# Kernel optimization log

Hardware: AMD Instinct MI355X
Metric: run time of the kernel (lower is better)

The kernel has to match this reference:

```python
import jax, jax.numpy as jnp
import numpy as np

B, T, D, H = 64, 512, 128, 512


def setup_inputs() -> dict:
    key = jax.random.key(0)
    ks = jax.random.split(key, 16)
    s_d = 1.0 / np.sqrt(D)
    s_h = 1.0 / np.sqrt(H)
    inp = {"x": jax.random.normal(ks[0], (B, T, D), dtype=jnp.float32)}
    # W* : [H, D] with bias; U* : [H, H] no bias (matches nn.Linear layout)
    inp["Wi_w"] = jax.random.uniform(ks[1], (H, D), minval=-s_d, maxval=s_d)
    inp["Wi_b"] = jax.random.uniform(ks[2], (H,), minval=-s_d, maxval=s_d)
    inp["Ui_w"] = jax.random.uniform(ks[3], (H, H), minval=-s_h, maxval=s_h)
    inp["Wf_w"] = jax.random.uniform(ks[4], (H, D), minval=-s_d, maxval=s_d)
    inp["Wf_b"] = jax.random.uniform(ks[5], (H,), minval=-s_d, maxval=s_d)
    inp["Uf_w"] = jax.random.uniform(ks[6], (H, H), minval=-s_h, maxval=s_h)
    inp["Wo_w"] = jax.random.uniform(ks[7], (H, D), minval=-s_d, maxval=s_d)
    inp["Wo_b"] = jax.random.uniform(ks[8], (H,), minval=-s_d, maxval=s_d)
    inp["Uo_w"] = jax.random.uniform(ks[9], (H, H), minval=-s_h, maxval=s_h)
    inp["Wg_w"] = jax.random.uniform(ks[10], (H, D), minval=-s_d, maxval=s_d)
    inp["Wg_b"] = jax.random.uniform(ks[11], (H,), minval=-s_d, maxval=s_d)
    inp["Ug_w"] = jax.random.uniform(ks[12], (H, H), minval=-s_h, maxval=s_h)
    inp["out_w"] = jax.random.uniform(ks[13], (1, H), minval=-s_h, maxval=s_h)
    inp["out_b"] = jnp.zeros((1,), dtype=jnp.float32)
    return inp


def _lstm_forward(x, Wi_w, Wi_b, Ui_w, Wf_w, Wf_b, Uf_w, Wo_w, Wo_b, Uo_w,
                  Wg_w, Wg_b, Ug_w, out_w, out_b):
    Bb = x.shape[0]
    Hh = Ui_w.shape[0]
    uf_d = jnp.diagonal(Uf_w)
    ui_d = jnp.diagonal(Ui_w)
    ug_d = jnp.diagonal(Ug_w)
    # Precompute input-side projections for all timesteps: [T, B, H]
    xi = (jnp.einsum('btd,hd->bth', x, Wi_w) + Wi_b).transpose(1, 0, 2)
    xf = (jnp.einsum('btd,hd->bth', x, Wf_w) + Wf_b).transpose(1, 0, 2)
    xo = (jnp.einsum('btd,hd->bth', x, Wo_w) + Wo_b).transpose(1, 0, 2)
    xg = (jnp.einsum('btd,hd->bth', x, Wg_w) + Wg_b).transpose(1, 0, 2)

    def step(carry, inp_t):
        h, c_prev = carry
        xi_t, xf_t, xo_t, xg_t = inp_t
        i = jax.nn.sigmoid(xi_t + h @ Ui_w.T)
        f = jax.nn.sigmoid(xf_t + h @ Uf_w.T)
        o = jax.nn.sigmoid(xo_t + h @ Uo_w.T)
        g = jnp.tanh(xg_t + h @ Ug_w.T)  # ln disabled -> identity
        c = f * c_prev + i * g
        tanh_c = jnp.tanh(c)
        h_new = o * tanh_c
        y = h_new @ out_w.T + out_b
        e = o * (1.0 - tanh_c ** 2)
        cdiag = (c_prev * (f * (1.0 - f)) * uf_d
                 + i * (1.0 - g ** 2) * ug_d
                 + g * (i * (1.0 - i)) * ui_d)
        return (h_new, c), (y, h_new, f, e, cdiag)

    h0 = jnp.zeros((Bb, Hh), dtype=x.dtype)
    c0 = jnp.zeros((Bb, Hh), dtype=x.dtype)
    _, (ys, hs, fs, es, cds) = jax.lax.scan(step, (h0, c0), (xi, xf, xo, xg))
    # scan outputs are time-major [T, B, ...] -> [B, T, ...]
    to_bt = lambda a: a.transpose(1, 0, 2)
    return to_bt(ys), to_bt(hs), to_bt(fs), to_bt(es), to_bt(cds)


def reference(x, Wi_w, Wi_b, Ui_w, Wf_w, Wf_b, Uf_w, Wo_w, Wo_b, Uo_w,
              Wg_w, Wg_b, Ug_w, out_w, out_b):
    return _lstm_forward(x, Wi_w, Wi_b, Ui_w, Wf_w, Wf_b, Uf_w, Wo_w, Wo_b,
                         Uo_w, Wg_w, Wg_b, Ug_w, out_w, out_b)
```

## Files before the change

### kernel.cpp

```cpp
#include <hip/hip_runtime.h>
#include <math.h>

#define BB 64
#define TT 512
#define DD 128
#define HH 512
#define NROW 16
#define NCG 16
#define NWG 256
#define TAGM 511u

#define LOADB2(d0,d1, ptr)                                                    \
  asm volatile("global_load_dword %0, %2, off sc0 sc1\n\t"                    \
               "global_load_dword %1, %2, off offset:2048 sc0 sc1"            \
               : "=v"(d0), "=v"(d1) : "v"(ptr) : "memory")

#define BARRIER_LGKM() asm volatile("s_waitcnt lgkmcnt(0)\n\ts_barrier" ::: "memory")

__global__ __launch_bounds__(256) void uT2_kernel(
    const float* __restrict__ Ui_w, const float* __restrict__ Uf_w,
    const float* __restrict__ Uo_w, const float* __restrict__ Ug_w,
    float* __restrict__ utT2)
{
    const int cg = blockIdx.x;
    for (int idx = threadIdx.x; idx < HH * 128; idx += 256) {
        const int k = idx >> 7, ii = idx & 127;
        const int l = ii >> 1, d = ii & 1;
        const int j = cg * 32 + (l & 31);
        const int g = ((l >> 5) << 1) + d;
        const float* U = (g == 0) ? Ui_w : (g == 1) ? Uf_w : (g == 2) ? Uo_w : Ug_w;
        utT2[((size_t)cg * HH + k) * 128 + ii] = U[(size_t)j * HH + k];
    }
}

__global__ __launch_bounds__(512, 2) void lstm_persist(
    const float* __restrict__ utT2,
    const float* __restrict__ Ui_w, const float* __restrict__ Uf_w,
    const float* __restrict__ Ug_w,
    const float* __restrict__ x,
    const float* __restrict__ Wi_w, const float* __restrict__ Wi_b,
    const float* __restrict__ Wf_w, const float* __restrict__ Wf_b,
    const float* __restrict__ Wo_w, const float* __restrict__ Wo_b,
    const float* __restrict__ Wg_w, const float* __restrict__ Wg_b,
    float* __restrict__ b_i, float* __restrict__ b_f,
    float* __restrict__ b_o, float* __restrict__ b_g,
    unsigned* __restrict__ hpub,
    int* __restrict__ flags)
{
    __shared__ float  hlds[8][4][64];
    __shared__ float2 red2[2][8][2][128];
    __shared__ float  xps[2][4][128];
    __shared__ float  shout[2][4][128];
    __shared__ float  xlds[2][4][128];

    const int tid  = threadIdx.x;
    const int w    = tid >> 6;
    const int lane = tid & 63;
    const int wg   = blockIdx.x;
    const int r    = wg & 15;
    const int cg   = wg >> 4;
    const int k0   = w << 6;

    float2 u2[64];
    {
        const float* ub = utT2 + ((size_t)cg * HH + k0) * 128 + 2 * lane;
        #pragma unroll
        for (int k = 0; k < 64; ++k) u2[k] = *(const float2*)(ub + (size_t)k * 128);
    }

    float creg = 0.f, uid = 0.f, ufd = 0.f, ugd = 0.f;
    int jjg = 0, gb = 0;
    if (tid < 128) {
        jjg = cg * 32 + (tid & 31);
        gb  = r * 4 + (tid >> 5);
        uid = Ui_w[(size_t)jjg * HH + jjg];
        ufd = Uf_w[(size_t)jjg * HH + jjg];
        ugd = Ug_w[(size_t)jjg * HH + jjg];
    }

    float4 wreg[16];
    float  wbias = 0.f;
    const int ga = (w >= 4) ? (w - 4) : 0;
    if (w >= 4) {
        const int col = lane & 31, dh = lane >> 5;
        const float* Ws = (ga == 0) ? Wi_w : (ga == 1) ? Wf_w : (ga == 2) ? Wo_w : Wg_w;
        const float* Bs = (ga == 0) ? Wi_b : (ga == 1) ? Wf_b : (ga == 2) ? Wo_b : Wg_b;
        const float* base = Ws + (size_t)(cg * 32 + col) * DD + dh * 64;
        #pragma unroll
        for (int k4 = 0; k4 < 16; ++k4) wreg[k4] = *(const float4*)(base + k4 * 4);
        wbias = Bs[cg * 32 + col];
    }

    if (w == 4) {
        const int bx = lane >> 4, c8 = lane & 15;
        #pragma unroll
        for (int u = 0; u < 2; ++u) {
            const float* xs = x + ((size_t)(r * 4 + bx) * TT + u) * DD + c8 * 8;
            *(float4*)&xlds[u][bx][c8 * 8]     = *(const float4*)(xs);
            *(float4*)&xlds[u][bx][c8 * 8 + 4] = *(const float4*)(xs + 4);
        }
    }
    __syncthreads();
    if (w >= 4) {
        const int col = lane & 31, dh = lane >> 5;
        #pragma unroll
        for (int b = 0; b < 4; ++b) {
            float a = 0.f;
            #pragma unroll
            for (int k4 = 0; k4 < 16; ++k4) {
                const float4 xv = *(const float4*)&xlds[0][b][dh * 64 + k4 * 4];
                const float4 ww = wreg[k4];
                a = fmaf(xv.x, ww.x, a); a = fmaf(xv.y, ww.y, a);
                a = fmaf(xv.z, ww.z, a); a = fmaf(xv.w, ww.w, a);
            }
            const float full = a + __shfl_xor(a, 32);
            if (lane < 32) xps[0][ga][b * 32 + col] = full + wbias;
        }
    }
    __syncthreads();

    for (int t = 0; t < TT; ++t) {
        const int p  = t & 1;
        const int np = p ^ 1;
        const unsigned tg = (unsigned)t & TAGM;

        unsigned hv[4];
        const char* hb = (const char*)hpub
                       + ((size_t)(p * 64 + r * 4) * HH + k0 + lane) * 4;
        for (;;) {
            LOADB2(hv[0], hv[1], hb);
            LOADB2(hv[2], hv[3], hb + 4096);
            asm volatile("s_waitcnt vmcnt(0)" ::: "memory");
            __builtin_amdgcn_sched_barrier(0);
            unsigned bad = 0;
            #pragma unroll
            for (int b = 0; b < 4; ++b) bad |= (hv[b] ^ tg) & TAGM;
            if (__all(bad == 0)) break;
            const int* fb = &flags[p * (NROW * NCG) + r * NCG];
            for (;;) {
                const int fv = __hip_atomic_load(&fb[lane & 15], __ATOMIC_RELAXED,
                                                 __HIP_MEMORY_SCOPE_AGENT);
                if (__all(fv >= t)) break;
                __builtin_amdgcn_s_sleep(2);
            }
        }

        #pragma unroll
        for (int b = 0; b < 4; ++b)
            hlds[w][b][lane] = __uint_as_float(hv[b] & ~TAGM);

        float acc[4][2];
        #pragma unroll
        for (int b = 0; b < 4; ++b) { acc[b][0] = 0.f; acc[b][1] = 0.f; }
        #pragma unroll
        for (int k4 = 0; k4 < 16; ++k4) {
            #pragma unroll
            for (int b = 0; b < 4; ++b) {
                const float4 h4 = *(const float4*)&hlds[w][b][k4 * 4];
                const float2 ua = u2[k4 * 4 + 0];
                const float2 ub = u2[k4 * 4 + 1];
                const float2 uc = u2[k4 * 4 + 2];
                const float2 ud = u2[k4 * 4 + 3];
                acc[b][0] = fmaf(h4.x, ua.x, acc[b][0]);
                acc[b][1] = fmaf(h4.x, ua.y, acc[b][1]);
                acc[b][0] = fmaf(h4.y, ub.x, acc[b][0]);
                acc[b][1] = fmaf(h4.y, ub.y, acc[b][1]);
                acc[b][0] = fmaf(h4.z, uc.x, acc[b][0]);
                acc[b][1] = fmaf(h4.z, uc.y, acc[b][1]);
                acc[b][0] = fmaf(h4.w, ud.x, acc[b][0]);
                acc[b][1] = fmaf(h4.w, ud.y, acc[b][1]);
            }
        }
        {
            const int col = lane & 31, gp = lane >> 5;
            #pragma unroll
            for (int b = 0; b < 4; ++b)
                red2[p][w][gp][b * 32 + col] = make_float2(acc[b][0], acc[b][1]);
        }
        BARRIER_LGKM();

        if (w < 2) {
            float s0 = 0.f, s1 = 0.f, s2 = 0.f, s3 = 0.f;
            #pragma unroll
            for (int ww = 0; ww < 8; ++ww) {
                const float2 a = red2[p][ww][0][tid];
                const float2 b = red2[p][ww][1][tid];
                s0 += a.x; s1 += a.y; s2 += b.x; s3 += b.y;
            }
            const float pi = xps[p][0][tid] + s0;
            const float pf = xps[p][1][tid] + s1;
            const float po = xps[p][2][tid] + s2;
            const float pg = xps[p][3][tid] + s3;

            const float ig = __fdividef(1.f, 1.f + __expf(-pi));
            const float fg = __fdividef(1.f, 1.f + __expf(-pf));
            const float og = __fdividef(1.f, 1.f + __expf(-po));
            const float tgg = __expf(-2.f * fmaxf(pg, -40.f));
            const float gg = __fdividef(1.f - tgg, 1.f + tgg);

            const float cp = creg;
            const float c  = fg * cp + ig * gg;
            creg = c;
            const float tc = __expf(-2.f * fmaxf(c, -40.f));
            const float th = __fdividef(1.f - tc, 1.f + tc);
            const float h  = og * th;
            const float e  = og * (1.f - th * th);
            const float cd = cp * (fg * (1.f - fg)) * ufd
                           + ig * (1.f - gg * gg) * ugd
                           + gg * (ig * (1.f - ig)) * uid;

            const unsigned pk = (__float_as_uint(h) & ~TAGM)
                              | ((unsigned)(t + 1) & TAGM);
            unsigned* dp = hpub + ((size_t)np * 64 + gb) * HH + jjg;
            asm volatile("global_store_dword %0, %1, off sc0 sc1"
                         :: "v"(dp), "v"(pk) : "memory");
            if (tid == 0)
                __hip_atomic_store(&flags[np * (NROW * NCG) + r * NCG + cg], t + 1,
                                   __ATOMIC_RELAXED, __HIP_MEMORY_SCOPE_AGENT);

            shout[p][0][tid] = h;
            shout[p][1][tid] = fg;
            shout[p][2][tid] = e;
            shout[p][3][tid] = cd;
        } else if (w < 4) {
            if (t > 0) {
                const int a2  = ((w - 2) << 1) | (lane >> 5);
                const int i32 = lane & 31;
                float* dstb = (a2 == 0) ? b_i : (a2 == 1) ? b_f
                            : (a2 == 2) ? b_o : b_g;
                const float4 v = *(const float4*)&shout[np][a2][i32 * 4];
                *(float4*)(dstb + ((size_t)(r * 4 + (i32 >> 3)) * TT + (t - 1)) * HH
                           + cg * 32 + (i32 & 7) * 4) = v;
            }
        } else {
            if (t + 1 < TT) {
                const int col = lane & 31, dh = lane >> 5;
                #pragma unroll
                for (int b = 0; b < 4; ++b) {
                    float a = 0.f;
                    #pragma unroll
                    for (int k4 = 0; k4 < 16; ++k4) {
                        const float4 xv = *(const float4*)&xlds[np][b][dh * 64 + k4 * 4];
                        const float4 ww = wreg[k4];
                        a = fmaf(xv.x, ww.x, a); a = fmaf(xv.y, ww.y, a);
                        a = fmaf(xv.z, ww.z, a); a = fmaf(xv.w, ww.w, a);
                    }
                    const float full = a + __shfl_xor(a, 32);
                    if (lane < 32) xps[np][ga][b * 32 + col] = full + wbias;
                }
            }
            if (w == 4 && t + 2 < TT) {
                const int bx = lane >> 4, c8 = lane & 15;
                const float* xs = x + ((size_t)(r * 4 + bx) * TT + (t + 2)) * DD + c8 * 8;
                *(float4*)&xlds[p][bx][c8 * 8]     = *(const float4*)(xs);
                *(float4*)&xlds[p][bx][c8 * 8 + 4] = *(const float4*)(xs + 4);
            }
        }
    }

    __syncthreads();
    if (w == 2 || w == 3) {
        const int a2  = ((w - 2) << 1) | (lane >> 5);
        const int i32 = lane & 31;
        float* dstb = (a2 == 0) ? b_i : (a2 == 1) ? b_f : (a2 == 2) ? b_o : b_g;
        const float4 v = *(const float4*)&shout[1][a2][i32 * 4];
        *(float4*)(dstb + ((size_t)(r * 4 + (i32 >> 3)) * TT + (TT - 1)) * HH
                   + cg * 32 + (i32 & 7) * 4) = v;
    }
}

__global__ __launch_bounds__(256) void lstm_y(
    const float* __restrict__ hs, const float* __restrict__ out_w,
    const float* __restrict__ out_b, float* __restrict__ ys)
{
    const int wave = threadIdx.x >> 6;
    const int lane = threadIdx.x & 63;
    const int rr = blockIdx.x * 4 + wave;

    const float4* hv = (const float4*)(hs + (size_t)rr * HH);
    const float4* wv = (const float4*)out_w;
    float acc = 0.f;
    #pragma unroll
    for (int i = 0; i < 2; ++i) {
        float4 h4 = hv[lane * 2 + i];
        float4 w4 = wv[lane * 2 + i];
        acc += h4.x * w4.x + h4.y * w4.y + h4.z * w4.z + h4.w * w4.w;
    }
    #pragma unroll
    for (int m = 32; m >= 1; m >>= 1) acc += __shfl_xor(acc, m, 64);
    if (lane == 0) ys[rr] = acc + out_b[0];
}

extern "C" void kernel_launch(void* const* d_in, const int* in_sizes, int n_in,
                              void* d_out, int out_size, void* d_ws, size_t ws_size,
                              hipStream_t stream)
{
    const float* x    = (const float*)d_in[0];
    const float* Wi_w = (const float*)d_in[1];
    const float* Wi_b = (const float*)d_in[2];
    const float* Ui_w = (const float*)d_in[3];
    const float* Wf_w = (const float*)d_in[4];
    const float* Wf_b = (const float*)d_in[5];
    const float* Uf_w = (const float*)d_in[6];
    const float* Wo_w = (const float*)d_in[7];
    const float* Wo_b = (const float*)d_in[8];
    const float* Uo_w = (const float*)d_in[9];
    const float* Wg_w = (const float*)d_in[10];
    const float* Wg_b = (const float*)d_in[11];
    const float* Ug_w = (const float*)d_in[12];
    const float* out_w = (const float*)d_in[13];
    const float* out_b = (const float*)d_in[14];

    float* ys  = (float*)d_out;
    float* hs  = ys + (size_t)BB * TT;
    float* fs  = hs + (size_t)BB * TT * HH;
    float* es  = fs + (size_t)BB * TT * HH;
    float* cds = es + (size_t)BB * TT * HH;

    unsigned* hpub  = (unsigned*)d_ws;
    int*      flags = (int*)(hpub + (size_t)2 * BB * HH);
    float*    utT2  = (float*)(flags + 2 * NROW * NCG);

    hipMemsetAsync(d_ws, 0,
                   (size_t)2 * BB * HH * sizeof(unsigned)
                   + (size_t)2 * NROW * NCG * sizeof(int), stream);

    uT2_kernel<<<NCG, 256, 0, stream>>>(Ui_w, Uf_w, Uo_w, Ug_w, utT2);

    lstm_persist<<<NWG, 512, 0, stream>>>(utT2, Ui_w, Uf_w, Ug_w,
                                          x, Wi_w, Wi_b, Wf_w, Wf_b,
                                          Wo_w, Wo_b, Wg_w, Wg_b,
                                          hs, fs, es, cds, hpub, flags);

    lstm_y<<<(BB * TT) / 4, 256, 0, stream>>>(hs, out_w, out_b, ys);
}
```

Before: 3.154 ms.

## Add XCC-local fast path for hidden-state exchange with system-scope fallback

```diff
diff --git a/kernel.cpp b/kernel.cpp
--- a/kernel.cpp
+++ b/kernel.cpp
@@ -9,8 +9,13 @@
 #define NCG 16
 #define NWG 256
 #define TAGM 511u
-
-#define LOADB2(d0,d1, ptr)                                                    \
+#define AG __ATOMIC_RELAXED, __HIP_MEMORY_SCOPE_AGENT
+
+#define LOADF2(d0,d1, ptr)                                                    \
+  asm volatile("global_load_dword %0, %2, off sc0\n\t"                        \
+               "global_load_dword %1, %2, off offset:2048 sc0"                \
+               : "=v"(d0), "=v"(d1) : "v"(ptr) : "memory")
+#define LOADS2(d0,d1, ptr)                                                    \
   asm volatile("global_load_dword %0, %2, off sc0 sc1\n\t"                    \
                "global_load_dword %1, %2, off offset:2048 sc0 sc1"            \
                : "=v"(d0), "=v"(d1) : "v"(ptr) : "memory")
@@ -45,13 +50,15 @@
     float* __restrict__ b_i, float* __restrict__ b_f,
     float* __restrict__ b_o, float* __restrict__ b_g,
     unsigned* __restrict__ hpub,
-    int* __restrict__ flags)
+    unsigned* __restrict__ hpub2,
+    int* __restrict__ hand)
 {
     __shared__ float  hlds[8][4][64];
     __shared__ float2 red2[2][8][2][128];
     __shared__ float  xps[2][4][128];
     __shared__ float  shout[2][4][128];
     __shared__ float  xlds[2][4][128];
+    __shared__ int    fastsh;
 
     const int tid  = threadIdx.x;
     const int w    = tid >> 6;
@@ -66,6 +73,24 @@
         const float* ub = utT2 + ((size_t)cg * HH + k0) * 128 + 2 * lane;
         #pragma unroll
         for (int k = 0; k < 64; ++k) u2[k] = *(const float2*)(ub + (size_t)k * 128);
+    }
+
+    {
+        const int xcc = __builtin_amdgcn_s_getreg(63508) & 0xf;
+        if (tid == 0) {
+            __hip_atomic_store(&hand[2 + wg], 0x100 | xcc, AG);
+            __hip_atomic_fetch_or((unsigned*)&hand[1], 1u << (xcc & 31), AG);
+            __hip_atomic_fetch_add(&hand[0], 1, AG);
+            while (__hip_atomic_load(&hand[0], AG) < NWG)
+                __builtin_amdgcn_s_sleep(8);
+            int ok = (xcc < 8) ? 1 : 0;
+            const int my = 0x100 | xcc;
+            for (int m = 0; m < NCG; ++m)
+                ok &= (__hip_atomic_load(&hand[2 + r + 16 * m], AG) == my) ? 1 : 0;
+            const unsigned msk = (unsigned)__hip_atomic_load(&hand[1], AG);
+            ok &= (__popc(msk) >= 2) ? 1 : 0;
+            fastsh = ok;
+        }
     }
 
     float creg = 0.f, uid = 0.f, ufd = 0.f, ugd = 0.f;
@@ -101,6 +126,8 @@
         }
     }
     __syncthreads();
+    const bool fastp = (fastsh != 0);
+    int mode = fastp ? 0 : 1;
     if (w >= 4) {
         const int col = lane & 31, dh = lane >> 5;
         #pragma unroll
@@ -124,30 +151,46 @@
         const int np = p ^ 1;
         const unsigned tg = (unsigned)t & TAGM;
 
-        unsigned hv[4];
-        const char* hb = (const char*)hpub
-                       + ((size_t)(p * 64 + r * 4) * HH + k0 + lane) * 4;
-        for (;;) {
-            LOADB2(hv[0], hv[1], hb);
-            LOADB2(hv[2], hv[3], hb + 4096);
-            asm volatile("s_waitcnt vmcnt(0)" ::: "memory");
-            __builtin_amdgcn_sched_barrier(0);
-            unsigned bad = 0;
-            #pragma unroll
-            for (int b = 0; b < 4; ++b) bad |= (hv[b] ^ tg) & TAGM;
-            if (__all(bad == 0)) break;
-            const int* fb = &flags[p * (NROW * NCG) + r * NCG];
-            for (;;) {
-                const int fv = __hip_atomic_load(&fb[lane & 15], __ATOMIC_RELAXED,
-                                                 __HIP_MEMORY_SCOPE_AGENT);
-                if (__all(fv >= t)) break;
-                __builtin_amdgcn_s_sleep(2);
-            }
-        }
-
-        #pragma unroll
-        for (int b = 0; b < 4; ++b)
-            hlds[w][b][lane] = __uint_as_float(hv[b] & ~TAGM);
+        if (t == 0) {
+            #pragma unroll
+            for (int b = 0; b < 4; ++b) hlds[w][b][lane] = 0.f;
+        } else {
+            unsigned hv[4];
+            const size_t hoff = ((size_t)(p * 64 + r * 4) * HH + k0 + lane) * 4;
+            bool got = false;
+            if (mode == 0) {
+                const char* hb = (const char*)hpub + hoff;
+                for (int tries = 0; tries < 1024; ++tries) {
+                    LOADF2(hv[0], hv[1], hb);
+                    LOADF2(hv[2], hv[3], hb + 4096);
+                    asm volatile("s_waitcnt vmcnt(0)" ::: "memory");
+                    __builtin_amdgcn_sched_barrier(0);
+                    unsigned bad = 0;
+                    #pragma unroll
+                    for (int b = 0; b < 4; ++b) bad |= (hv[b] ^ tg) & TAGM;
+                    if (__all(bad == 0)) { got = true; break; }
+                    __builtin_amdgcn_s_sleep(1);
+                }
+                if (!got) mode = 1;
+            }
+            if (!got) {
+                const char* hb = (const char*)hpub2 + hoff;
+                for (;;) {
+                    LOADS2(hv[0], hv[1], hb);
+                    LOADS2(hv[2], hv[3], hb + 4096);
+                    asm volatile("s_waitcnt vmcnt(0)" ::: "memory");
+                    __builtin_amdgcn_sched_barrier(0);
+                    unsigned bad = 0;
+                    #pragma unroll
+                    for (int b = 0; b < 4; ++b) bad |= (hv[b] ^ tg) & TAGM;
+                    if (__all(bad == 0)) break;
+                    __builtin_amdgcn_s_sleep(2);
+                }
+            }
+            #pragma unroll
+            for (int b = 0; b < 4; ++b)
+                hlds[w][b][lane] = __uint_as_float(hv[b] & ~TAGM);
+        }
 
         float acc[4][2];
         #pragma unroll
@@ -180,6 +223,7 @@
         BARRIER_LGKM();
 
         if (w < 2) {
+            __builtin_amdgcn_s_setprio(1);
             float s0 = 0.f, s1 = 0.f, s2 = 0.f, s3 = 0.f;
             #pragma unroll
             for (int ww = 0; ww < 8; ++ww) {
@@ -204,20 +248,28 @@
             const float tc = __expf(-2.f * fmaxf(c, -40.f));
             const float th = __fdividef(1.f - tc, 1.f + tc);
             const float h  = og * th;
+
+            const unsigned pk = (__float_as_uint(h) & ~TAGM)
+                              | ((unsigned)(t + 1) & TAGM);
+            const size_t po2 = (size_t)np * 64 * HH + (size_t)gb * HH + jjg;
+            if (fastp) {
+                unsigned* dp  = hpub  + po2;
+                unsigned* dp2 = hpub2 + po2;
+                asm volatile("global_store_dword %0, %1, off sc0"
+                             :: "v"(dp), "v"(pk) : "memory");
+                asm volatile("global_store_dword %0, %1, off sc0 sc1"
+                             :: "v"(dp2), "v"(pk) : "memory");
+            } else {
+                unsigned* dp2 = hpub2 + po2;
+                asm volatile("global_store_dword %0, %1, off sc0 sc1"
+                             :: "v"(dp2), "v"(pk) : "memory");
+            }
+            __builtin_amdgcn_s_setprio(0);
+
             const float e  = og * (1.f - th * th);
             const float cd = cp * (fg * (1.f - fg)) * ufd
                            + ig * (1.f - gg * gg) * ugd
                            + gg * (ig * (1.f - ig)) * uid;
-
-            const unsigned pk = (__float_as_uint(h) & ~TAGM)
-                              | ((unsigned)(t + 1) & TAGM);
-            unsigned* dp = hpub + ((size_t)np * 64 + gb) * HH + jjg;
-            asm volatile("global_store_dword %0, %1, off sc0 sc1"
-                         :: "v"(dp), "v"(pk) : "memory");
-            if (tid == 0)
-                __hip_atomic_store(&flags[np * (NROW * NCG) + r * NCG + cg], t + 1,
-                                   __ATOMIC_RELAXED, __HIP_MEMORY_SCOPE_AGENT);
-
             shout[p][0][tid] = h;
             shout[p][1][tid] = fg;
             shout[p][2][tid] = e;
@@ -318,19 +370,20 @@
     float* cds = es + (size_t)BB * TT * HH;
 
     unsigned* hpub  = (unsigned*)d_ws;
-    int*      flags = (int*)(hpub + (size_t)2 * BB * HH);
-    float*    utT2  = (float*)(flags + 2 * NROW * NCG);
+    unsigned* hpub2 = hpub + (size_t)2 * BB * HH;
+    int*      hand  = (int*)(hpub2 + (size_t)2 * BB * HH);
+    float*    utT2  = (float*)(hand + 1024);
 
     hipMemsetAsync(d_ws, 0,
-                   (size_t)2 * BB * HH * sizeof(unsigned)
-                   + (size_t)2 * NROW * NCG * sizeof(int), stream);
+                   (size_t)4 * BB * HH * sizeof(unsigned) + 1024 * sizeof(int),
+                   stream);
 
     uT2_kernel<<<NCG, 256, 0, stream>>>(Ui_w, Uf_w, Uo_w, Ug_w, utT2);
 
     lstm_persist<<<NWG, 512, 0, stream>>>(utT2, Ui_w, Uf_w, Ug_w,
                                           x, Wi_w, Wi_b, Wf_w, Wf_b,
                                           Wo_w, Wo_b, Wg_w, Wg_b,
-                                          hs, fs, es, cds, hpub, flags);
+                                          hs, fs, es, cds, hpub, hpub2, hand);
 
     lstm_y<<<(BB * TT) / 4, 256, 0, stream>>>(hs, out_w, out_b, ys);
 }
```

After: 4.674 ms. 1.48x slower.

## Interleave published h as x4 vectors, drop flag polling, prioritize publish

Applied to the files above, without the earlier changes.

```diff
diff --git a/kernel.cpp b/kernel.cpp
--- a/kernel.cpp
+++ b/kernel.cpp
@@ -10,10 +10,11 @@
 #define NWG 256
 #define TAGM 511u
 
-#define LOADB2(d0,d1, ptr)                                                    \
-  asm volatile("global_load_dword %0, %2, off sc0 sc1\n\t"                    \
-               "global_load_dword %1, %2, off offset:2048 sc0 sc1"            \
-               : "=v"(d0), "=v"(d1) : "v"(ptr) : "memory")
+typedef unsigned uint4v __attribute__((ext_vector_type(4)));
+
+#define LOADX4(d, ptr)                                                        \
+  asm volatile("global_load_dwordx4 %0, %1, off sc0 sc1"                      \
+               : "=v"(d) : "v"(ptr) : "memory")
 
 #define BARRIER_LGKM() asm volatile("s_waitcnt lgkmcnt(0)\n\ts_barrier" ::: "memory")
 
@@ -44,8 +45,7 @@
     const float* __restrict__ Wg_w, const float* __restrict__ Wg_b,
     float* __restrict__ b_i, float* __restrict__ b_f,
     float* __restrict__ b_o, float* __restrict__ b_g,
-    unsigned* __restrict__ hpub,
-    int* __restrict__ flags)
+    unsigned* __restrict__ hpub)
 {
     __shared__ float  hlds[8][4][64];
     __shared__ float2 red2[2][8][2][128];
@@ -69,10 +69,10 @@
     }
 
     float creg = 0.f, uid = 0.f, ufd = 0.f, ugd = 0.f;
-    int jjg = 0, gb = 0;
+    int jjg = 0, b4 = 0;
     if (tid < 128) {
         jjg = cg * 32 + (tid & 31);
-        gb  = r * 4 + (tid >> 5);
+        b4  = tid >> 5;
         uid = Ui_w[(size_t)jjg * HH + jjg];
         ufd = Uf_w[(size_t)jjg * HH + jjg];
         ugd = Ug_w[(size_t)jjg * HH + jjg];
@@ -124,30 +124,26 @@
         const int np = p ^ 1;
         const unsigned tg = (unsigned)t & TAGM;
 
-        unsigned hv[4];
-        const char* hb = (const char*)hpub
-                       + ((size_t)(p * 64 + r * 4) * HH + k0 + lane) * 4;
-        for (;;) {
-            LOADB2(hv[0], hv[1], hb);
-            LOADB2(hv[2], hv[3], hb + 4096);
-            asm volatile("s_waitcnt vmcnt(0)" ::: "memory");
-            __builtin_amdgcn_sched_barrier(0);
-            unsigned bad = 0;
-            #pragma unroll
-            for (int b = 0; b < 4; ++b) bad |= (hv[b] ^ tg) & TAGM;
-            if (__all(bad == 0)) break;
-            const int* fb = &flags[p * (NROW * NCG) + r * NCG];
+        if (t == 0) {
+            #pragma unroll
+            for (int b = 0; b < 4; ++b) hlds[w][b][lane] = 0.f;
+        } else {
+            uint4v hv;
+            const char* hb = (const char*)hpub
+                           + (((size_t)(p * NROW + r) * HH + k0 + lane) << 4);
             for (;;) {
-                const int fv = __hip_atomic_load(&fb[lane & 15], __ATOMIC_RELAXED,
-                                                 __HIP_MEMORY_SCOPE_AGENT);
-                if (__all(fv >= t)) break;
-                __builtin_amdgcn_s_sleep(2);
-            }
-        }
-
-        #pragma unroll
-        for (int b = 0; b < 4; ++b)
-            hlds[w][b][lane] = __uint_as_float(hv[b] & ~TAGM);
+                LOADX4(hv, hb);
+                asm volatile("s_waitcnt vmcnt(0)" ::: "memory");
+                __builtin_amdgcn_sched_barrier(0);
+                unsigned bad = 0;
+                #pragma unroll
+                for (int b = 0; b < 4; ++b) bad |= (hv[b] ^ tg) & TAGM;
+                if (__all(bad == 0)) break;
+            }
+            #pragma unroll
+            for (int b = 0; b < 4; ++b)
+                hlds[w][b][lane] = __uint_as_float(hv[b] & ~TAGM);
+        }
 
         float acc[4][2];
         #pragma unroll
@@ -180,6 +176,7 @@
         BARRIER_LGKM();
 
         if (w < 2) {
+            __builtin_amdgcn_s_setprio(1);
             float s0 = 0.f, s1 = 0.f, s2 = 0.f, s3 = 0.f;
             #pragma unroll
             for (int ww = 0; ww < 8; ++ww) {
@@ -204,20 +201,18 @@
             const float tc = __expf(-2.f * fmaxf(c, -40.f));
             const float th = __fdividef(1.f - tc, 1.f + tc);
             const float h  = og * th;
+
+            const unsigned pk = (__float_as_uint(h) & ~TAGM)
+                              | ((unsigned)(t + 1) & TAGM);
+            unsigned* dp = hpub + (((size_t)(np * NROW + r) * HH + jjg) << 2) + b4;
+            asm volatile("global_store_dword %0, %1, off sc0 sc1"
+                         :: "v"(dp), "v"(pk) : "memory");
+            __builtin_amdgcn_s_setprio(0);
+
             const float e  = og * (1.f - th * th);
             const float cd = cp * (fg * (1.f - fg)) * ufd
                            + ig * (1.f - gg * gg) * ugd
                            + gg * (ig * (1.f - ig)) * uid;
-
-            const unsigned pk = (__float_as_uint(h) & ~TAGM)
-                              | ((unsigned)(t + 1) & TAGM);
-            unsigned* dp = hpub + ((size_t)np * 64 + gb) * HH + jjg;
-            asm volatile("global_store_dword %0, %1, off sc0 sc1"
-                         :: "v"(dp), "v"(pk) : "memory");
-            if (tid == 0)
-                __hip_atomic_store(&flags[np * (NROW * NCG) + r * NCG + cg], t + 1,
-                                   __ATOMIC_RELAXED, __HIP_MEMORY_SCOPE_AGENT);
-
             shout[p][0][tid] = h;
             shout[p][1][tid] = fg;
             shout[p][2][tid] = e;
@@ -317,20 +312,17 @@
     float* es  = fs + (size_t)BB * TT * HH;
     float* cds = es + (size_t)BB * TT * HH;
 
-    unsigned* hpub  = (unsigned*)d_ws;
-    int*      flags = (int*)(hpub + (size_t)2 * BB * HH);
-    float*    utT2  = (float*)(flags + 2 * NROW * NCG);
-
-    hipMemsetAsync(d_ws, 0,
-                   (size_t)2 * BB * HH * sizeof(unsigned)
-                   + (size_t)2 * NROW * NCG * sizeof(int), stream);
+    unsigned* hpub = (unsigned*)d_ws;
+    float*    utT2 = (float*)(hpub + (size_t)2 * NROW * HH * 4);
+
+    hipMemsetAsync(d_ws, 0, (size_t)2 * NROW * HH * 4 * sizeof(unsigned), stream);
 
     uT2_kernel<<<NCG, 256, 0, stream>>>(Ui_w, Uf_w, Uo_w, Ug_w, utT2);
 
     lstm_persist<<<NWG, 512, 0, stream>>>(utT2, Ui_w, Uf_w, Ug_w,
                                           x, Wi_w, Wi_b, Wf_w, Wf_b,
                                           Wo_w, Wo_b, Wg_w, Wg_b,
-                                          hs, fs, es, cds, hpub, flags);
+                                          hs, fs, es, cds, hpub);
 
     lstm_y<<<(BB * TT) / 4, 256, 0, stream>>>(hs, out_w, out_b, ys);
 }
```

Measured after the change: 2.525 ms (median of 2 runs). -19.9%, faster.
